# Kernel optimization log

Measured on AMD Instinct MI355X. Metric: run time of the kernel, lower is better.

Reference implementation:

```python
import jax, jax.numpy as jnp
import numpy as np

B, H, W = 64, 14, 14
DIM, NH, LORA = 768, 12, 4
HD = DIM // NH  # 64


def setup_inputs() -> dict:
    key = jax.random.key(0)
    ks = jax.random.split(key, 12)
    s = 0.02
    return {
        "x": jax.random.normal(ks[0], (B, H, W, DIM), dtype=jnp.float32),
        "qkv_w": jax.random.normal(ks[1], (3 * DIM, DIM), dtype=jnp.float32) * s,
        "qkv_b": jax.random.normal(ks[2], (3 * DIM,), dtype=jnp.float32) * s,
        "proj_w": jax.random.normal(ks[3], (DIM, DIM), dtype=jnp.float32) * s,
        "proj_b": jax.random.normal(ks[4], (DIM,), dtype=jnp.float32) * s,
        "la_q": jax.random.normal(ks[5], (LORA, DIM), dtype=jnp.float32) * s,
        "lb_q": jax.random.normal(ks[6], (DIM, LORA), dtype=jnp.float32) * s,
        "la_v": jax.random.normal(ks[7], (LORA, DIM), dtype=jnp.float32) * s,
        "lb_v": jax.random.normal(ks[8], (DIM, LORA), dtype=jnp.float32) * s,
        "rel_pos_h": jax.random.normal(ks[9], (2 * H - 1, HD), dtype=jnp.float32) * s,
        "rel_pos_w": jax.random.normal(ks[10], (2 * W - 1, HD), dtype=jnp.float32) * s,
    }


def reference(x, qkv_w, qkv_b, proj_w, proj_b, la_q, lb_q, la_v, lb_v, rel_pos_h, rel_pos_w):
    b, h, w, c = x.shape
    nh, hd = NH, c // NH
    scale = hd ** -0.5

    # qkv projection with LoRA deltas on q and v
    qkv = x @ qkv_w.T + qkv_b                       # (b,h,w,3c)
    new_q = (x @ la_q.T) @ lb_q.T                   # (b,h,w,c)
    new_v = (x @ la_v.T) @ lb_v.T
    qkv = qkv.at[..., :c].add(new_q)
    qkv = qkv.at[..., 2 * c:].add(new_v)

    qkv = qkv.reshape(b, h * w, 3, nh, hd).transpose(2, 0, 3, 1, 4)
    qkv = qkv.reshape(3, b * nh, h * w, hd)
    q, k, v = qkv[0], qkv[1], qkv[2]

    attn = jnp.einsum('bqd,bkd->bqk', q * scale, k)  # (b*nh, hw, hw)

    # decomposed relative position bias; q_size == k_size so no interpolation
    idx_h = jnp.arange(h)[:, None] - jnp.arange(h)[None, :] + (h - 1)
    idx_w = jnp.arange(w)[:, None] - jnp.arange(w)[None, :] + (w - 1)
    Rh = rel_pos_h[idx_h]                            # (h,h,hd)
    Rw = rel_pos_w[idx_w]                            # (w,w,hd)
    r_q = q.reshape(b * nh, h, w, hd)
    rel_h = jnp.einsum('bhwc,hkc->bhwk', r_q, Rh)    # (b*nh,h,w,h)
    rel_w = jnp.einsum('bhwc,wkc->bhwk', r_q, Rw)    # (b*nh,h,w,w)
    attn = (attn.reshape(b * nh, h, w, h, w)
            + rel_h[:, :, :, :, None]
            + rel_w[:, :, :, None, :]).reshape(b * nh, h * w, h * w)

    attn = jax.nn.softmax(attn, axis=-1)
    out = jnp.einsum('bqk,bkd->bqd', attn, v)        # (b*nh, hw, hd)
    out = out.reshape(b, nh, h, w, hd).transpose(0, 2, 3, 1, 4).reshape(b, h, w, c)
    return out @ proj_w.T + proj_b
```

## Files before the change

kernel.cpp:

```cpp
#include <hip/hip_runtime.h>
#include <stdint.h>

#define DIM   768
#define NH    12
#define HD    64
#define NT    196
#define M_ROWS 12544

typedef __attribute__((ext_vector_type(8))) short bf16x8;
typedef __attribute__((ext_vector_type(4))) float f32x4;

__device__ __forceinline__ float b2f(short s) {
  union { unsigned u; float f; } c;
  c.u = ((unsigned)(unsigned short)s) << 16;
  return c.f;
}
__device__ __forceinline__ short f2b(float f) {
  union { float f; unsigned u; } c; c.f = f;
  unsigned u = c.u;
  u += 0x7fffu + ((u >> 16) & 1u);
  return (short)(u >> 16);
}

__device__ __forceinline__ f32x4 mfma16(bf16x8 a, bf16x8 b, f32x4 c) {
  return __builtin_amdgcn_mfma_f32_16x16x32_bf16(a, b, c, 0, 0, 0);
}

__device__ __forceinline__ void g2lds16(const short* g, short* l) {
  __builtin_amdgcn_global_load_lds(
      (const __attribute__((address_space(1))) void*)g,
      (__attribute__((address_space(3))) void*)l, 16, 0, 0);
}

struct CvtArgs { const float* src[5]; int n4[5]; int off[5]; };

__global__ __launch_bounds__(256) void k_cvt(CvtArgs a, short* __restrict__ dst) {
  const int tid = blockIdx.x * 256 + threadIdx.x;
  const int stride = gridDim.x * 256;
  #pragma unroll
  for (int s = 0; s < 5; ++s) {
    const float4* sp = (const float4*)a.src[s];
    short4* dp = (short4*)(dst + a.off[s]);
    const int n4 = a.n4[s];
    for (int i = tid; i < n4; i += stride) {
      float4 v = sp[i];
      short4 o = { f2b(v.x), f2b(v.y), f2b(v.z), f2b(v.w) };
      dp[i] = o;
    }
  }
}

__global__ __launch_bounds__(256) void k_lora_xa(
    const float* __restrict__ x, const float* __restrict__ la_q,
    const float* __restrict__ la_v, float* __restrict__ xa)
{
  __shared__ float sla[8][DIM];
  const int tid = threadIdx.x;
  for (int i = tid; i < 8 * DIM; i += 256) {
    int j = i / DIM, c = i - j * DIM;
    sla[j][c] = (j < 4) ? la_q[j * DIM + c] : la_v[(j - 4) * DIM + c];
  }
  __syncthreads();
  const int lane = tid & 63, wid = tid >> 6;
  const int m = blockIdx.x * 4 + wid;
  const float4* xr = (const float4*)(x + (size_t)m * DIM);
  float s[8] = {};
  #pragma unroll
  for (int i = 0; i < 3; ++i) {
    float4 xv = xr[lane + 64 * i];
    int c = (lane + 64 * i) * 4;
    #pragma unroll
    for (int j = 0; j < 8; ++j)
      s[j] += xv.x * sla[j][c] + xv.y * sla[j][c + 1]
            + xv.z * sla[j][c + 2] + xv.w * sla[j][c + 3];
  }
  #pragma unroll
  for (int j = 0; j < 8; ++j) {
    #pragma unroll
    for (int off = 32; off; off >>= 1) s[j] += __shfl_xor(s[j], off);
  }
  if (lane == 0) {
    float* o = xa + m * 8;
    #pragma unroll
    for (int j = 0; j < 8; ++j) o[j] = s[j];
  }
}

template<int EPI>
__global__ __launch_bounds__(256) void k_gemm(
    const short* __restrict__ A, const short* __restrict__ B,
    const float* __restrict__ bias, const float* __restrict__ xa,
    const float* __restrict__ lb_q, const float* __restrict__ lb_v,
    short* __restrict__ out, float* __restrict__ outf)
{
  constexpr int K = DIM;
  __shared__ short sA[128 * 32];
  __shared__ short sB[128 * 32];
  const int tid = threadIdx.x, lane = tid & 63, wid = tid >> 6;
  const int rm0 = blockIdx.x * 128, cn0 = blockIdx.y * 128;
  const int wm = (wid >> 1) * 64, wn = (wid & 1) * 64;
  const int fr = lane & 15, fg = lane >> 4;
  f32x4 acc[4][4] = {};
  const short* ga = A + (size_t)(rm0 + (tid >> 2)) * K + (tid & 3) * 8;
  const short* gb = B + (size_t)(cn0 + (tid >> 2)) * K + (tid & 3) * 8;
  short* lA = sA + wid * 512;
  short* lB = sB + wid * 512;

  for (int kt = 0; kt < K; kt += 32) {
    g2lds16(ga + kt, lA);
    g2lds16(ga + 64 * K + kt, lA + 2048);
    g2lds16(gb + kt, lB);
    g2lds16(gb + 64 * K + kt, lB + 2048);
    __syncthreads();
    bf16x8 af[4], bg[4];
    #pragma unroll
    for (int i = 0; i < 4; ++i)
      af[i] = *(const bf16x8*)&sA[(wm + i * 16 + fr) * 32 + fg * 8];
    #pragma unroll
    for (int j = 0; j < 4; ++j)
      bg[j] = *(const bf16x8*)&sB[(wn + j * 16 + fr) * 32 + fg * 8];
    #pragma unroll
    for (int i = 0; i < 4; ++i)
      #pragma unroll
      for (int j = 0; j < 4; ++j)
        acc[i][j] = mfma16(af[i], bg[j], acc[i][j]);
    __syncthreads();
  }

  int ncol[4]; float biasv[4];
  #pragma unroll
  for (int j = 0; j < 4; ++j) {
    ncol[j] = cn0 + wn + j * 16 + fr;
    biasv[j] = bias[ncol[j]];
  }

  if (EPI == 0) {
    const int reg = cn0 / DIM;
    float lb[4][4];
    if (reg != 1) {
      const float* lbt = (reg == 0) ? lb_q : lb_v;
      #pragma unroll
      for (int j = 0; j < 4; ++j) {
        int ni = ncol[j] - reg * DIM;
        #pragma unroll
        for (int l = 0; l < 4; ++l) lb[j][l] = lbt[ni * 4 + l];
      }
    }
    #pragma unroll
    for (int i = 0; i < 4; ++i) {
      #pragma unroll
      for (int r = 0; r < 4; ++r) {
        int m = rm0 + wm + i * 16 + fg * 4 + r;
        int b_i = m / NT, p = m - b_i * NT;
        float xv0 = 0, xv1 = 0, xv2 = 0, xv3 = 0;
        if (reg != 1) {
          const float* xp = xa + m * 8 + (reg == 2 ? 4 : 0);
          xv0 = xp[0]; xv1 = xp[1]; xv2 = xp[2]; xv3 = xp[3];
        }
        #pragma unroll
        for (int j = 0; j < 4; ++j) {
          float val = acc[i][j][r] + biasv[j];
          if (reg != 1)
            val += xv0 * lb[j][0] + xv1 * lb[j][1] + xv2 * lb[j][2] + xv3 * lb[j][3];
          int ni = ncol[j] - reg * DIM;
          int head = ni >> 6, d = ni & 63;
          out[(size_t)reg * (M_ROWS * DIM)
              + ((size_t)(b_i * NH + head) * NT + p) * HD + d] = f2b(val);
        }
      }
    }
  } else {
    #pragma unroll
    for (int i = 0; i < 4; ++i)
      #pragma unroll
      for (int r = 0; r < 4; ++r) {
        int m = rm0 + wm + i * 16 + fg * 4 + r;
        #pragma unroll
        for (int j = 0; j < 4; ++j)
          outf[(size_t)m * DIM + ncol[j]] = acc[i][j][r] + biasv[j];
      }
  }
}

__global__ __launch_bounds__(256) void k_attn(
    const short* __restrict__ qb, const short* __restrict__ kb,
    const short* __restrict__ vb, const short* __restrict__ rph,
    const short* __restrict__ rpw, short* __restrict__ ao)
{
  __shared__ short vst[64][216];
  __shared__ short pwb[4][16][208];
  __shared__ short relh[NT * 14];
  __shared__ short relw[NT * 14];
  const int tid = threadIdx.x, lane = tid & 63, wid = tid >> 6;
  const int fr = lane & 15, fg = lane >> 4;
  const int bh = blockIdx.x;
  const int b_i = bh / NH, head = bh - b_i * NH;
  const short* q0 = qb + (size_t)bh * NT * HD;
  const short* k0 = kb + (size_t)bh * NT * HD;
  const short* v0 = vb + (size_t)bh * NT * HD;

  for (int i = tid; i < 64 * 20; i += 256) {
    int d = i / 20, c = 196 + (i - (i / 20) * 20);
    vst[d][c] = 0;
  }
  for (int t = tid; t < NT * 8; t += 256) {
    int p = t >> 3, d0 = (t & 7) * 8;
    bf16x8 vv = *(const bf16x8*)(v0 + p * HD + d0);
    #pragma unroll
    for (int j = 0; j < 8; ++j) vst[d0 + j][p] = vv[j];
  }
  for (int job = wid; job < 28; job += 4) {
    const int isW = job >= 14 ? 1 : 0;
    const int fx = isW ? job - 14 : job;
    const int qrow = isW ? fr * 14 + fx : fx * 14 + fr;
    const bool aok = fr < 14;
    const short* rp = isW ? rpw : rph;
    int ridx = fx - fr + 13;
    ridx = ridx < 0 ? 0 : (ridx > 26 ? 26 : ridx);
    f32x4 racc = {0.f, 0.f, 0.f, 0.f};
    #pragma unroll
    for (int ks = 0; ks < 2; ++ks) {
      bf16x8 afr = {0,0,0,0,0,0,0,0};
      if (aok) afr = *(const bf16x8*)(q0 + qrow * HD + ks * 32 + fg * 8);
      bf16x8 bfr = *(const bf16x8*)(rp + ridx * HD + ks * 32 + fg * 8);
      racc = mfma16(afr, bfr, racc);
    }
    #pragma unroll
    for (int r = 0; r < 4; ++r) {
      int rr = fg * 4 + r;
      if (rr < 14 && fr < 14) {
        int p = isW ? rr * 14 + fx : fx * 14 + rr;
        (isW ? relw : relh)[p * 14 + fr] = f2b(racc[r]);
      }
    }
  }
  __syncthreads();

  const float scale = 0.125f;
  for (int t = wid; t < 13; t += 4) {
    const int m0 = t * 16;
    bf16x8 aq0 = {0,0,0,0,0,0,0,0}, aq1 = {0,0,0,0,0,0,0,0};
    {
      int arow = m0 + fr;
      if (arow < NT) {
        aq0 = *(const bf16x8*)(q0 + arow * HD + fg * 8);
        aq1 = *(const bf16x8*)(q0 + arow * HD + 32 + fg * 8);
      }
    }
    f32x4 sc[13] = {};
    #pragma unroll
    for (int ct = 0; ct < 13; ++ct) {
      int brow = ct * 16 + fr;
      bf16x8 bk0 = {0,0,0,0,0,0,0,0}, bk1 = {0,0,0,0,0,0,0,0};
      if (brow < NT) {
        bk0 = *(const bf16x8*)(k0 + brow * HD + fg * 8);
        bk1 = *(const bf16x8*)(k0 + brow * HD + 32 + fg * 8);
      }
      sc[ct] = mfma16(aq0, bk0, sc[ct]);
      sc[ct] = mfma16(aq1, bk1, sc[ct]);
    }
    float rmax[4] = {-1e30f, -1e30f, -1e30f, -1e30f};
    #pragma unroll
    for (int ct = 0; ct < 13; ++ct) {
      int kk = ct * 16 + fr;
      int kh = kk / 14, kw = kk - kh * 14;
      #pragma unroll
      for (int r = 0; r < 4; ++r) {
        int p = m0 + fg * 4 + r;
        float v;
        if (kk < NT && p < NT)
          v = sc[ct][r] * scale + b2f(relh[p * 14 + kh]) + b2f(relw[p * 14 + kw]);
        else
          v = -1e30f;
        sc[ct][r] = v;
        rmax[r] = fmaxf(rmax[r], v);
      }
    }
    #pragma unroll
    for (int r = 0; r < 4; ++r) {
      rmax[r] = fmaxf(rmax[r], __shfl_xor(rmax[r], 1));
      rmax[r] = fmaxf(rmax[r], __shfl_xor(rmax[r], 2));
      rmax[r] = fmaxf(rmax[r], __shfl_xor(rmax[r], 4));
      rmax[r] = fmaxf(rmax[r], __shfl_xor(rmax[r], 8));
    }
    float rsum[4] = {0.f, 0.f, 0.f, 0.f};
    #pragma unroll
    for (int ct = 0; ct < 13; ++ct)
      #pragma unroll
      for (int r = 0; r < 4; ++r) {
        float e = __expf(sc[ct][r] - rmax[r]);
        sc[ct][r] = e;
        rsum[r] += e;
      }
    #pragma unroll
    for (int r = 0; r < 4; ++r) {
      rsum[r] += __shfl_xor(rsum[r], 1);
      rsum[r] += __shfl_xor(rsum[r], 2);
      rsum[r] += __shfl_xor(rsum[r], 4);
      rsum[r] += __shfl_xor(rsum[r], 8);
    }
    #pragma unroll
    for (int ct = 0; ct < 13; ++ct)
      #pragma unroll
      for (int r = 0; r < 4; ++r)
        pwb[wid][fg * 4 + r][ct * 16 + fr] = f2b(sc[ct][r]);

    f32x4 oacc[4] = {};
    #pragma unroll
    for (int ks = 0; ks < 7; ++ks) {
      const bool hi = (ks == 6) && (fg >= 2);
      bf16x8 pa = {0,0,0,0,0,0,0,0};
      if (!hi) pa = *(const bf16x8*)&pwb[wid][fr][ks * 32 + fg * 8];
      #pragma unroll
      for (int dt = 0; dt < 4; ++dt) {
        bf16x8 vv = {0,0,0,0,0,0,0,0};
        if (!hi) vv = *(const bf16x8*)&vst[dt * 16 + fr][ks * 32 + fg * 8];
        oacc[dt] = mfma16(pa, vv, oacc[dt]);
      }
    }
    #pragma unroll
    for (int r = 0; r < 4; ++r) {
      int p = m0 + fg * 4 + r;
      if (p < NT) {
        float inv = 1.0f / rsum[r];
        size_t base = ((size_t)(b_i * NT + p)) * DIM + head * HD;
        #pragma unroll
        for (int dt = 0; dt < 4; ++dt)
          ao[base + dt * 16 + fr] = f2b(oacc[dt][r] * inv);
      }
    }
  }
}

extern "C" void kernel_launch(void* const* d_in, const int* in_sizes, int n_in,
                              void* d_out, int out_size, void* d_ws, size_t ws_size,
                              hipStream_t stream) {
  const float *x = nullptr, *qkv_w = nullptr, *qkv_b = nullptr,
              *proj_w = nullptr, *proj_b = nullptr, *rph = nullptr,
              *rpw = nullptr;
  const float* c3072[4] = {nullptr, nullptr, nullptr, nullptr};
  int n3072 = 0, n1728 = 0;
  for (int i = 0; i < n_in; ++i) {
    const float* p = (const float*)d_in[i];
    switch (in_sizes[i]) {
      case 9633792: x = p; break;
      case 1769472: qkv_w = p; break;
      case 2304:    qkv_b = p; break;
      case 589824:  proj_w = p; break;
      case 768:     proj_b = p; break;
      case 3072:    if (n3072 < 4) c3072[n3072++] = p; break;
      case 1728:    { if (n1728 == 0) rph = p; else rpw = p; ++n1728; } break;
      default: break;
    }
  }
  const bool alpha = (n_in >= 1 && in_sizes[n_in - 1] == 9633792);
  const float* la_q = c3072[0];
  const float* lb_q = alpha ? c3072[2] : c3072[1];
  const float* la_v = alpha ? c3072[1] : c3072[2];
  const float* lb_v = c3072[3];

  float* out = (float*)d_out;

  char* ws = (char*)d_ws;
  float* xa   = (float*)ws;
  short* qkvb = (short*)(ws + 401408);
  short* q_   = qkvb;
  short* k_   = qkvb + (size_t)M_ROWS * DIM;
  short* v_   = qkvb + (size_t)2 * M_ROWS * DIM;
  short* cvt  = (short*)(ws + 401408 + 57802752);
  short* xb      = cvt;
  short* qkv_wb  = cvt + 9633792;
  short* proj_wb = cvt + 11403264;
  short* rphb    = cvt + 11993088;
  short* rpwb    = cvt + 11994816;
  short* ao = xb;

  CvtArgs ca;
  ca.src[0] = x;      ca.n4[0] = 9633792 / 4;  ca.off[0] = 0;
  ca.src[1] = qkv_w;  ca.n4[1] = 1769472 / 4;  ca.off[1] = 9633792;
  ca.src[2] = proj_w; ca.n4[2] =  589824 / 4;  ca.off[2] = 11403264;
  ca.src[3] = rph;    ca.n4[3] =    1728 / 4;  ca.off[3] = 11993088;
  ca.src[4] = rpw;    ca.n4[4] =    1728 / 4;  ca.off[4] = 11994816;

  k_cvt<<<1024, 256, 0, stream>>>(ca, cvt);
  k_lora_xa<<<3136, 256, 0, stream>>>(x, la_q, la_v, xa);
  k_gemm<0><<<dim3(98, 18), 256, 0, stream>>>(xb, qkv_wb, qkv_b, xa, lb_q, lb_v,
                                              qkvb, nullptr);
  k_attn<<<768, 256, 0, stream>>>(q_, k_, v_, rphb, rpwb, ao);
  k_gemm<1><<<dim3(98, 6), 256, 0, stream>>>(ao, proj_wb, proj_b, nullptr, nullptr,
                                             nullptr, nullptr, out);
}
```

Measured before the change: 206.7 us.

## Triple-buffer LDS tiles in GEMM to overlap global loads with MFMA

```diff
diff --git a/kernel.cpp b/kernel.cpp
--- a/kernel.cpp
+++ b/kernel.cpp
@@ -94,8 +94,9 @@
     short* __restrict__ out, float* __restrict__ outf)
 {
   constexpr int K = DIM;
-  __shared__ short sA[128 * 32];
-  __shared__ short sB[128 * 32];
+  constexpr int NSTEP = K / 32;
+  __shared__ short sA[3][4096];
+  __shared__ short sB[3][4096];
   const int tid = threadIdx.x, lane = tid & 63, wid = tid >> 6;
   const int rm0 = blockIdx.x * 128, cn0 = blockIdx.y * 128;
   const int wm = (wid >> 1) * 64, wn = (wid & 1) * 64;
@@ -103,29 +104,44 @@
   f32x4 acc[4][4] = {};
   const short* ga = A + (size_t)(rm0 + (tid >> 2)) * K + (tid & 3) * 8;
   const short* gb = B + (size_t)(cn0 + (tid >> 2)) * K + (tid & 3) * 8;
-  short* lA = sA + wid * 512;
-  short* lB = sB + wid * 512;
-
-  for (int kt = 0; kt < K; kt += 32) {
-    g2lds16(ga + kt, lA);
-    g2lds16(ga + 64 * K + kt, lA + 2048);
-    g2lds16(gb + kt, lB);
-    g2lds16(gb + 64 * K + kt, lB + 2048);
-    __syncthreads();
+  const int lo = wid * 512;
+
+  #define STAGE(buf, kt)                                   \
+    do {                                                   \
+      g2lds16(ga + (kt),          &sA[buf][lo]);           \
+      g2lds16(ga + 64 * K + (kt), &sA[buf][2048 + lo]);    \
+      g2lds16(gb + (kt),          &sB[buf][lo]);           \
+      g2lds16(gb + 64 * K + (kt), &sB[buf][2048 + lo]);    \
+    } while (0)
+
+  STAGE(0, 0);
+  STAGE(1, 32);
+
+  for (int t = 0; t < NSTEP; ++t) {
+    if (t < NSTEP - 1) asm volatile("s_waitcnt vmcnt(4)" ::: "memory");
+    else               asm volatile("s_waitcnt vmcnt(0)" ::: "memory");
+    __builtin_amdgcn_s_barrier();
+    __builtin_amdgcn_sched_barrier(0);
+    if (t + 2 < NSTEP) {
+      int b2 = (t + 2) % 3;
+      STAGE(b2, (t + 2) * 32);
+    }
+    const short* lA = sA[t % 3];
+    const short* lB = sB[t % 3];
     bf16x8 af[4], bg[4];
     #pragma unroll
     for (int i = 0; i < 4; ++i)
-      af[i] = *(const bf16x8*)&sA[(wm + i * 16 + fr) * 32 + fg * 8];
+      af[i] = *(const bf16x8*)&lA[(wm + i * 16 + fr) * 32 + fg * 8];
     #pragma unroll
     for (int j = 0; j < 4; ++j)
-      bg[j] = *(const bf16x8*)&sB[(wn + j * 16 + fr) * 32 + fg * 8];
+      bg[j] = *(const bf16x8*)&lB[(wn + j * 16 + fr) * 32 + fg * 8];
     #pragma unroll
     for (int i = 0; i < 4; ++i)
       #pragma unroll
       for (int j = 0; j < 4; ++j)
         acc[i][j] = mfma16(af[i], bg[j], acc[i][j]);
-    __syncthreads();
-  }
+  }
+  #undef STAGE
 
   int ncol[4]; float biasv[4];
   #pragma unroll
```

Result: no change. 208.7 us (+0.9%).
